# Optimization experiments

Measured on AMD Instinct MI355X. Metric: run time of the kernel, lower is better.

The kernel has to match this reference:

```python
import jax, jax.numpy as jnp
import numpy as np

D = 256      # cfg.d_model
H = 8        # num heads
HID = D // H # head_outdim for hidden layers (32)
N = 16000    # nodes
E = 64000    # edges
NUM_GNN = 3  # cfg.num_gnn -> 2 hidden EGATConv layers + 1 final
SLOPE = 0.01 # F.leaky_relu default in DGL EGATConv


def setup_inputs() -> dict:
    key = jax.random.key(0)
    ks = jax.random.split(key, 8)
    inp = {
        "nfeat": jax.random.normal(ks[0], (N, D), jnp.float32),
        "efeat": jax.random.normal(ks[1], (E, D), jnp.float32),
        "src": jax.random.randint(ks[2], (E,), 0, N),
        "dst": jax.random.randint(ks[3], (E,), 0, N),
    }
    L = NUM_GNN - 1  # hidden layers, out_node = out_edge = HID per head
    kh = jax.random.split(ks[4], 5)
    s = 0.02
    inp["Wnode_h"] = jax.random.normal(kh[0], (L, D, H * HID), jnp.float32) * s
    inp["Wni_h"]   = jax.random.normal(kh[1], (L, D, H * HID), jnp.float32) * s
    inp["Wnj_h"]   = jax.random.normal(kh[2], (L, D, H * HID), jnp.float32) * s
    inp["Wfij_h"]  = jax.random.normal(kh[3], (L, D, H * HID), jnp.float32) * s
    inp["attn_h"]  = jax.random.normal(kh[4], (L, H, HID), jnp.float32) * s
    inp["bias_h"]  = jnp.zeros((L, H * HID), jnp.float32)
    kl = jax.random.split(ks[5], 5)
    inp["Wnode_l"] = jax.random.normal(kl[0], (D, H * D), jnp.float32) * s
    inp["Wni_l"]   = jax.random.normal(kl[1], (D, H * D), jnp.float32) * s
    inp["Wnj_l"]   = jax.random.normal(kl[2], (D, H * D), jnp.float32) * s
    inp["Wfij_l"]  = jax.random.normal(kl[3], (D, H * D), jnp.float32) * s
    inp["attn_l"]  = jax.random.normal(kl[4], (H, D), jnp.float32) * s
    inp["bias_l"]  = jnp.zeros((H * D,), jnp.float32)
    return inp


def _egat(n, f, src, dst, Wnode, Wni, Wnj, Wfij, attn, bias):
    """DGL EGATConv: edge-gated multi-head graph attention.
    n:[N,D] f:[E,D] attn:[H,od] -> (h_out:[N,H,od], f_out:[E,H,od])."""
    Hh, od = attn.shape
    # edge feature update: f_ni(u) + f_nj(v) + f_fij(e) + bias, leaky_relu
    f_out = (n @ Wni)[src] + (n @ Wnj)[dst] + f @ Wfij + bias  # [E, H*od]
    f_out = jax.nn.leaky_relu(f_out, SLOPE).reshape(-1, Hh, od)
    # attention logits + edge softmax grouped by destination node
    e = jnp.einsum('ehd,hd->eh', f_out, attn)                   # [E, H]
    m = jax.lax.stop_gradient(jax.ops.segment_max(e, dst, num_segments=N))
    ex = jnp.exp(e - m[dst])
    s = jax.ops.segment_sum(ex, dst, num_segments=N)
    a = ex / s[dst]                                             # [E, H]
    # message passing: u_mul_e + sum at dst
    h = (n @ Wnode).reshape(N, Hh, od)
    h_out = jax.ops.segment_sum(h[src] * a[..., None], dst, num_segments=N)
    return h_out, f_out


def reference(nfeat, efeat, src, dst,
              Wnode_h, Wni_h, Wnj_h, Wfij_h, attn_h, bias_h,
              Wnode_l, Wni_l, Wnj_l, Wfij_l, attn_l, bias_l):
    n, f = nfeat, efeat
    for l in range(Wnode_h.shape[0]):  # hidden layers: concat heads + ELU + residual
        tn, tf = _egat(n, f, src, dst, Wnode_h[l], Wni_h[l], Wnj_h[l],
                       Wfij_h[l], attn_h[l], bias_h[l])
        n = n + jax.nn.elu(tn.reshape(N, -1))  # reshape == concat over heads
        f = f + jax.nn.elu(tf.reshape(E, -1))
    # last layer: mean over heads + residual
    tn, tf = _egat(n, f, src, dst, Wnode_l, Wni_l, Wnj_l, Wfij_l, attn_l, bias_l)
    n = n + tn.mean(axis=1)
    f = f + tf.mean(axis=1)
    return n, f
```

## Files before the change

### kernel.cpp

```cpp
#include <hip/hip_runtime.h>

typedef unsigned short u16;
typedef __attribute__((ext_vector_type(4))) unsigned short u16x4;
typedef __attribute__((ext_vector_type(8))) unsigned short u16x8;
typedef __attribute__((ext_vector_type(4))) float f32x4;
typedef __attribute__((ext_vector_type(8))) __bf16 bf16x8;

#define NN 16000
#define NE 64000

__device__ __forceinline__ float bf2f(u16 b) {
  union { unsigned int u; float f; } v; v.u = ((unsigned int)b) << 16; return v.f;
}
__device__ __forceinline__ u16 f2bf(float x) {
  union { float f; unsigned int u; } v; v.f = x;
  unsigned int r = v.u + 0x7FFFu + ((v.u >> 16) & 1u);
  return (u16)(r >> 16);
}

__global__ void cast_init(const float* __restrict__ in, float* __restrict__ outf,
                          u16* __restrict__ outb, int n4) {
  for (int i = blockIdx.x * blockDim.x + threadIdx.x; i < n4; i += gridDim.x * blockDim.x) {
    f32x4 v = ((const f32x4*)in)[i];
    u16x4 b;
#pragma unroll
    for (int j = 0; j < 4; ++j) b[j] = f2bf(v[j]);
    ((f32x4*)outf)[i] = v;
    ((u16x4*)outb)[i] = b;
  }
}

__global__ void cast_bf(const float* __restrict__ in, u16* __restrict__ outb, int n4) {
  for (int i = blockIdx.x * blockDim.x + threadIdx.x; i < n4; i += gridDim.x * blockDim.x) {
    f32x4 v = ((const f32x4*)in)[i];
    u16x4 b;
#pragma unroll
    for (int j = 0; j < 4; ++j) b[j] = f2bf(v[j]);
    ((u16x4*)outb)[i] = b;
  }
}

__global__ void deg_hist(const int* __restrict__ dst, int* __restrict__ deg) {
  int e = blockIdx.x * 256 + threadIdx.x;
  if (e < NE) atomicAdd(&deg[dst[e]], 1);
}

__global__ __launch_bounds__(1024) void scan_deg(const int* __restrict__ deg,
                                                 int* __restrict__ row_ptr,
                                                 int* __restrict__ cursor) {
  __shared__ int lds[1024];
  int t = threadIdx.x;
  int base = t * 16;
  int v[16];
  int s = 0;
#pragma unroll
  for (int j = 0; j < 16; ++j) {
    int idx = base + j;
    v[j] = idx < NN ? deg[idx] : 0;
    s += v[j];
  }
  lds[t] = s;
  __syncthreads();
  for (int d = 1; d < 1024; d <<= 1) {
    int x = t >= d ? lds[t - d] : 0;
    __syncthreads();
    lds[t] += x;
    __syncthreads();
  }
  int run = lds[t] - s;
  for (int j = 0; j < 16; ++j) {
    int idx = base + j;
    if (idx < NN) { row_ptr[idx] = run; cursor[idx] = run; run += v[j]; }
  }
  if (t == 1023) row_ptr[NN] = run;
}

__global__ void csr_fill(const int* __restrict__ src, const int* __restrict__ dst,
                         int* __restrict__ cursor, int* __restrict__ cs_e,
                         int* __restrict__ cs_src) {
  int e = blockIdx.x * 256 + threadIdx.x;
  if (e >= NE) return;
  int pos = atomicAdd(&cursor[dst[e]], 1);
  cs_e[pos] = e;
  cs_src[pos] = src[e];
}

__global__ void transpose4(const float* __restrict__ W0, const float* __restrict__ W1,
                           const float* __restrict__ W2, const float* __restrict__ W3,
                           int ld, int osz, u16* __restrict__ WT) {
  __shared__ float t[16][17];
  int z = blockIdx.z;
  const float* W = z == 0 ? W0 : (z == 1 ? W1 : (z == 2 ? W2 : W3));
  u16* O = WT + (size_t)z * osz;
  int n0 = blockIdx.x * 16, k0 = blockIdx.y * 16;
  int tx = threadIdx.x, ty = threadIdx.y;
  t[ty][tx] = W[(size_t)(k0 + ty) * ld + n0 + tx];
  __syncthreads();
  O[(size_t)(n0 + ty) * 256 + k0 + tx] = f2bf(t[tx][ty]);
}

__global__ __launch_bounds__(256) void gemm_abt(
    const u16* __restrict__ A,
    const u16* __restrict__ BT0, const u16* __restrict__ BT1, const u16* __restrict__ BT2,
    u16* __restrict__ C0, u16* __restrict__ C1, u16* __restrict__ C2, int ldc) {
  const int bz = blockIdx.z;
  const u16* BT = bz == 0 ? BT0 : (bz == 1 ? BT1 : BT2);
  u16* C = bz == 0 ? C0 : (bz == 1 ? C1 : C2);
  const int nx = gridDim.x;
  const int nwg = nx * gridDim.y;
  int bid = blockIdx.y * nx + blockIdx.x;
  int q = nwg >> 3, r = nwg & 7;
  int xcd = bid & 7, idx = bid >> 3;
  int wg = (xcd < r) ? (xcd * (q + 1) + idx) : (r * (q + 1) + (xcd - r) * q + idx);
  const int m0 = (wg / nx) * 128;
  const int n0 = (wg % nx) * 128;
  __shared__ __attribute__((aligned(16))) char smem[69632];
  u16* lA = (u16*)smem;
  u16* lB = (u16*)(smem + 32768);
  const int tid = threadIdx.x;
  const int lane = tid & 63;
  const int wid = tid >> 6;
  const int wr = (wid >> 1) * 64;
  const int wc = (wid & 1) * 64;
  const int srow = tid >> 3;
  const int sdst = (tid & 7) * 8;
  const int ssrc = (((tid & 7) ^ (srow & 7))) * 8;
  const int sx = (lane >> 4) ^ (lane & 7);
  f32x4 acc[4][4] = {};
#define STAGE(buf, kb)                                                                         \
  {                                                                                            \
    _Pragma("unroll") for (int i = 0; i < 4; ++i) {                                            \
      const int row = srow + i * 32;                                                           \
      __builtin_amdgcn_global_load_lds(                                                        \
          (const __attribute__((address_space(1))) void*)(A + (size_t)(m0 + row) * 256 + (kb) + ssrc), \
          (__attribute__((address_space(3))) void*)(lA + (buf) * 8192 + row * 64 + sdst), 16, 0, 0); \
      __builtin_amdgcn_global_load_lds(                                                        \
          (const __attribute__((address_space(1))) void*)(BT + (size_t)(n0 + row) * 256 + (kb) + ssrc), \
          (__attribute__((address_space(3))) void*)(lB + (buf) * 8192 + row * 64 + sdst), 16, 0, 0); \
    }                                                                                          \
  }
  STAGE(0, 0)
  __syncthreads();
#pragma unroll
  for (int t = 0; t < 4; ++t) {
    if (t < 3) STAGE((t + 1) & 1, (t + 1) * 64)
    const u16* pA = lA + (t & 1) * 8192;
    const u16* pB = lB + (t & 1) * 8192;
#pragma unroll
    for (int kk = 0; kk < 2; ++kk) {
      const int sw = ((kk << 2) ^ sx) * 8;
      bf16x8 af[4], bfr[4];
#pragma unroll
      for (int m = 0; m < 4; ++m)
        af[m] = *(const bf16x8*)(pA + (wr + m * 16 + (lane & 15)) * 64 + sw);
#pragma unroll
      for (int n = 0; n < 4; ++n)
        bfr[n] = *(const bf16x8*)(pB + (wc + n * 16 + (lane & 15)) * 64 + sw);
#pragma unroll
      for (int m = 0; m < 4; ++m)
#pragma unroll
        for (int n = 0; n < 4; ++n)
          acc[m][n] = __builtin_amdgcn_mfma_f32_16x16x32_bf16(af[m], bfr[n], acc[m][n], 0, 0, 0);
    }
    __syncthreads();
  }
#undef STAGE
  const int cr = (lane >> 4) * 4;
  const int cc = lane & 15;
  float* stg = (float*)smem + wid * (64 * 68);
#pragma unroll
  for (int m = 0; m < 4; ++m)
#pragma unroll
    for (int n = 0; n < 4; ++n)
#pragma unroll
      for (int j = 0; j < 4; ++j)
        stg[(m * 16 + cr + j) * 68 + n * 16 + cc] = acc[m][n][j];
  const int rr = lane >> 3;
  const int c0 = (lane & 7) * 8;
#pragma unroll
  for (int p = 0; p < 8; ++p) {
    int row = p * 8 + rr;
    f32x4 v0 = *(const f32x4*)(stg + row * 68 + c0);
    f32x4 v1 = *(const f32x4*)(stg + row * 68 + c0 + 4);
    u16x8 o;
#pragma unroll
    for (int i = 0; i < 4; ++i) { o[i] = f2bf(v0[i]); o[4 + i] = f2bf(v1[i]); }
    *(u16x8*)(&C[(size_t)(m0 + wr + row) * ldc + (n0 + wc + c0)]) = o;
  }
}

__global__ __launch_bounds__(256) void edge_hidden(
    const u16* __restrict__ t_ni, const u16* __restrict__ t_nj, const u16* __restrict__ fW,
    const int* __restrict__ src, const int* __restrict__ dst,
    const float* __restrict__ bias, const float* __restrict__ attn,
    u16* __restrict__ f_bf, float* __restrict__ exb) {
  int e = blockIdx.x * 4 + (threadIdx.x >> 6);
  if (e >= NE) return;
  int lane = threadIdx.x & 63;
  int is = src[e], id = dst[e];
  int c = lane * 4;
  u16x4 va = *(const u16x4*)(t_ni + (size_t)is * 256 + c);
  u16x4 vb = *(const u16x4*)(t_nj + (size_t)id * 256 + c);
  u16x4 vc = *(const u16x4*)(fW + (size_t)e * 256 + c);
  f32x4 vbi = *(const f32x4*)(bias + c);
  int h = lane >> 3;
  f32x4 vat = *(const f32x4*)(attn + h * 32 + (lane & 7) * 4);
  size_t idx0 = (size_t)e * 256 + c;
  u16x4 fo = *(u16x4*)(f_bf + idx0);
  float part = 0.f;
#pragma unroll
  for (int j = 0; j < 4; ++j) {
    float y = bf2f(va[j]) + bf2f(vb[j]) + bf2f(vc[j]) + vbi[j];
    y = y > 0.f ? y : 0.01f * y;
    part += y * vat[j];
    float el = y > 0.f ? y : expm1f(y);
    fo[j] = f2bf(bf2f(fo[j]) + el);
  }
  *(u16x4*)(f_bf + idx0) = fo;
  part += __shfl_xor(part, 1);
  part += __shfl_xor(part, 2);
  part += __shfl_xor(part, 4);
  part = fminf(fmaxf(part, -30.f), 30.f);
  if ((lane & 7) == 0) exb[(size_t)e * 8 + h] = expf(part);
}

__global__ __launch_bounds__(256) void node_gather_hidden(
    const u16* __restrict__ t_node, const int* __restrict__ row_ptr,
    const int* __restrict__ cs_e, const int* __restrict__ cs_src,
    const float* __restrict__ exb, float* __restrict__ n_cur, u16* __restrict__ n_bf) {
  int node = blockIdx.x * 4 + (threadIdx.x >> 6);
  if (node >= NN) return;
  int lane = threadIdx.x & 63;
  int c = lane * 4, h = lane >> 3;
  int beg = row_ptr[node], end = row_ptr[node + 1];
  float denom = 0.f;
  float acc[4] = {0.f, 0.f, 0.f, 0.f};
  for (int p = beg; p < end; ++p) {
    float a = exb[(size_t)cs_e[p] * 8 + h];
    denom += a;
    u16x4 hv = *(const u16x4*)(t_node + (size_t)cs_src[p] * 256 + c);
#pragma unroll
    for (int j = 0; j < 4; ++j) acc[j] += a * bf2f(hv[j]);
  }
  float inv = denom > 0.f ? 1.f / denom : 0.f;
  size_t i0 = (size_t)node * 256 + c;
  f32x4 nv = *(f32x4*)(n_cur + i0);
  u16x4 bv;
#pragma unroll
  for (int j = 0; j < 4; ++j) {
    float t = acc[j] * inv;
    t = t > 0.f ? t : expm1f(t);
    nv[j] += t;
    bv[j] = f2bf(nv[j]);
  }
  *(f32x4*)(n_cur + i0) = nv;
  *(u16x4*)(n_bf + i0) = bv;
}

__global__ __launch_bounds__(256) void edge_final_all(
    int e0, int nech, const u16* __restrict__ t_ni, const u16* __restrict__ t_nj,
    const u16* __restrict__ fWc, const int* __restrict__ src, const int* __restrict__ dst,
    const float* __restrict__ bias, const float* __restrict__ attn,
    const u16* __restrict__ f_bf, float* __restrict__ out_f, float* __restrict__ exb) {
  int ec = blockIdx.x * 4 + (threadIdx.x >> 6);
  if (ec >= nech) return;
  int e = e0 + ec;
  int lane = threadIdx.x & 63;
  int is = src[e], id = dst[e];
  int c = lane * 4;
  float total[4] = {0.f, 0.f, 0.f, 0.f};
#pragma unroll
  for (int h = 0; h < 8; ++h) {
    u16x4 va = *(const u16x4*)(t_ni + (size_t)is * 2048 + h * 256 + c);
    u16x4 vb = *(const u16x4*)(t_nj + (size_t)id * 2048 + h * 256 + c);
    u16x4 vc = *(const u16x4*)(fWc + (size_t)ec * 2048 + h * 256 + c);
    f32x4 vbi = *(const f32x4*)(bias + h * 256 + c);
    f32x4 vat = *(const f32x4*)(attn + h * 256 + c);
    float part = 0.f;
#pragma unroll
    for (int j = 0; j < 4; ++j) {
      float y = bf2f(va[j]) + bf2f(vb[j]) + bf2f(vc[j]) + vbi[j];
      y = y > 0.f ? y : 0.01f * y;
      part += y * vat[j];
      total[j] += 0.125f * y;
    }
#pragma unroll
    for (int m = 1; m < 64; m <<= 1) part += __shfl_xor(part, m);
    part = fminf(fmaxf(part, -30.f), 30.f);
    if (lane == 0) exb[(size_t)e * 8 + h] = expf(part);
  }
  size_t i0 = (size_t)e * 256 + c;
  u16x4 fs = *(const u16x4*)(f_bf + i0);
  f32x4 o;
#pragma unroll
  for (int j = 0; j < 4; ++j) o[j] = bf2f(fs[j]) + total[j];
  *(f32x4*)(out_f + i0) = o;
}

__global__ __launch_bounds__(256) void node_gather_final_all(
    const u16* __restrict__ t_node, const int* __restrict__ row_ptr,
    const int* __restrict__ cs_e, const int* __restrict__ cs_src,
    const float* __restrict__ exb, const float* __restrict__ n_cur,
    float* __restrict__ out_n) {
  int node = blockIdx.x * 4 + (threadIdx.x >> 6);
  if (node >= NN) return;
  int lane = threadIdx.x & 63;
  int c = lane * 4;
  int beg = row_ptr[node], end = row_ptr[node + 1];
  float dh[8] = {};
  float acc[8][4] = {};
  for (int p = beg; p < end; ++p) {
    int e = cs_e[p];
    int s = cs_src[p];
    const u16* rowb = t_node + (size_t)s * 2048;
    const float* eb = exb + (size_t)e * 8;
    float a[8];
    u16x4 rv[8];
#pragma unroll
    for (int h = 0; h < 8; ++h) {
      a[h] = eb[h];
      rv[h] = *(const u16x4*)(rowb + h * 256 + c);
    }
#pragma unroll
    for (int h = 0; h < 8; ++h) {
      dh[h] += a[h];
#pragma unroll
      for (int j = 0; j < 4; ++j) acc[h][j] += a[h] * bf2f(rv[h][j]);
    }
  }
  float total[4] = {0.f, 0.f, 0.f, 0.f};
#pragma unroll
  for (int h = 0; h < 8; ++h) {
    float inv = dh[h] > 0.f ? 0.125f / dh[h] : 0.f;
#pragma unroll
    for (int j = 0; j < 4; ++j) total[j] += acc[h][j] * inv;
  }
  size_t i0 = (size_t)node * 256 + c;
  f32x4 nv = *(const f32x4*)(n_cur + i0);
#pragma unroll
  for (int j = 0; j < 4; ++j) nv[j] += total[j];
  *(f32x4*)(out_n + i0) = nv;
}

extern "C" void kernel_launch(void* const* d_in, const int* in_sizes, int n_in,
                              void* d_out, int out_size, void* d_ws, size_t ws_size,
                              hipStream_t stream) {
  const float* nfeat   = (const float*)d_in[0];
  const float* efeat   = (const float*)d_in[1];
  const int*   src     = (const int*)d_in[2];
  const int*   dst     = (const int*)d_in[3];
  const float* Wnode_h = (const float*)d_in[4];
  const float* Wni_h   = (const float*)d_in[5];
  const float* Wnj_h   = (const float*)d_in[6];
  const float* Wfij_h  = (const float*)d_in[7];
  const float* attn_h  = (const float*)d_in[8];
  const float* bias_h  = (const float*)d_in[9];
  const float* Wnode_l = (const float*)d_in[10];
  const float* Wni_l   = (const float*)d_in[11];
  const float* Wnj_l   = (const float*)d_in[12];
  const float* Wfij_l  = (const float*)d_in[13];
  const float* attn_l  = (const float*)d_in[14];
  const float* bias_l  = (const float*)d_in[15];

  char* ws = (char*)d_ws;
  size_t off = 0;
  auto alloc = [&](size_t b) { char* p = ws + off; off += (b + 255) & ~(size_t)255; return p; };
  float* n_cur = (float*)alloc((size_t)NN * 256 * 4);
  u16* n_bf    = (u16*)alloc((size_t)NN * 256 * 2);
  u16* f_bf    = (u16*)alloc((size_t)NE * 256 * 2);
  u16* t_ni    = (u16*)alloc((size_t)NN * 2048 * 2);
  u16* t_nj    = (u16*)alloc((size_t)NN * 2048 * 2);
  u16* t_node  = (u16*)alloc((size_t)NN * 2048 * 2);
  float* exb   = (float*)alloc((size_t)NE * 8 * 4);
  u16* WT      = (u16*)alloc((size_t)4 * 65536 * 2);
  u16* WTF     = (u16*)alloc((size_t)4 * 524288 * 2);
  int* deg     = (int*)alloc((size_t)NN * 4);
  int* cursor  = (int*)alloc((size_t)NN * 4);
  int* row_ptr = (int*)alloc((size_t)(NN + 1) * 4);
  int* cs_e    = (int*)alloc((size_t)NE * 4);
  int* cs_src  = (int*)alloc((size_t)NE * 4);
  int ech;
  u16* fW;
  size_t fw_big = (size_t)16000 * 2048 * 2;
  size_t fw_small = (size_t)NE * 256 * 2;
  if (off + fw_big <= ws_size) { ech = 16000; fW = (u16*)alloc(fw_big); }
  else                         { ech = 6400;  fW = (u16*)alloc(fw_small); }

  u16* WT_node = WT;
  u16* WT_ni   = WT + 65536;
  u16* WT_nj   = WT + 2 * 65536;
  u16* WT_fij  = WT + 3 * 65536;
  u16* WTF_node = WTF;
  u16* WTF_ni   = WTF + (size_t)1 * 524288;
  u16* WTF_nj   = WTF + (size_t)2 * 524288;
  u16* WTF_fij  = WTF + (size_t)3 * 524288;

  float* out_n = (float*)d_out;
  float* out_f = out_n + (size_t)NN * 256;

  hipMemsetAsync(deg, 0, (size_t)NN * 4, stream);
  deg_hist<<<(NE + 255) / 256, 256, 0, stream>>>(dst, deg);
  scan_deg<<<1, 1024, 0, stream>>>(deg, row_ptr, cursor);
  csr_fill<<<(NE + 255) / 256, 256, 0, stream>>>(src, dst, cursor, cs_e, cs_src);

  cast_init<<<1024, 256, 0, stream>>>(nfeat, n_cur, n_bf, NN * 256 / 4);
  cast_bf<<<2048, 256, 0, stream>>>(efeat, f_bf, NE * 256 / 4);

  for (int l = 0; l < 2; ++l) {
    transpose4<<<dim3(16, 16, 4), dim3(16, 16), 0, stream>>>(
        Wnode_h + (size_t)l * 65536, Wni_h + (size_t)l * 65536,
        Wnj_h + (size_t)l * 65536, Wfij_h + (size_t)l * 65536, 256, 65536, WT);
    gemm_abt<<<dim3(2, 125, 3), 256, 0, stream>>>(n_bf, WT_ni, WT_nj, WT_node,
                                                  t_ni, t_nj, t_node, 256);
    gemm_abt<<<dim3(2, 500, 1), 256, 0, stream>>>(f_bf, WT_fij, WT_fij, WT_fij,
                                                  fW, fW, fW, 256);
    edge_hidden<<<16000, 256, 0, stream>>>(t_ni, t_nj, fW, src, dst,
        bias_h + (size_t)l * 256, attn_h + (size_t)l * 256, f_bf, exb);
    node_gather_hidden<<<4000, 256, 0, stream>>>(t_node, row_ptr, cs_e, cs_src, exb, n_cur, n_bf);
  }

  transpose4<<<dim3(128, 16, 4), dim3(16, 16), 0, stream>>>(
      Wnode_l, Wni_l, Wnj_l, Wfij_l, 2048, 524288, WTF);
  gemm_abt<<<dim3(16, 125, 3), 256, 0, stream>>>(n_bf, WTF_ni, WTF_nj, WTF_node,
                                                 t_ni, t_nj, t_node, 2048);
  for (int e0 = 0; e0 < NE; e0 += ech) {
    const u16* Ac = f_bf + (size_t)e0 * 256;
    gemm_abt<<<dim3(16, ech / 128, 1), 256, 0, stream>>>(Ac, WTF_fij, WTF_fij, WTF_fij,
                                                         fW, fW, fW, 2048);
    edge_final_all<<<ech / 4, 256, 0, stream>>>(e0, ech, t_ni, t_nj, fW, src, dst,
                                                bias_l, attn_l, f_bf, out_f, exb);
  }
  node_gather_final_all<<<4000, 256, 0, stream>>>(t_node, row_ptr, cs_e, cs_src,
                                                  exb, n_cur, out_n);
}
```

Baseline: 669.1 us.

## Shrink GEMM LDS tiles to K=32 and write outputs directly from registers

The bf16 GEMM now stages K in 32-wide slices instead of 64, cutting shared memory from about 68KB to 32KB per block and requesting 4 blocks per CU through launch bounds. The MFMA operand order is swapped so each lane holds four consecutive output columns, which lets results be written straight from registers as 8-byte stores without the LDS staging epilogue. The aim is higher occupancy and less epilogue LDS traffic, at the cost of twice as many K iterations and barriers, narrower global stores, and possible register pressure under the tighter bound.

```diff
diff --git a/kernel.cpp b/kernel.cpp
--- a/kernel.cpp
+++ b/kernel.cpp
@@ -99,7 +99,7 @@
   O[(size_t)(n0 + ty) * 256 + k0 + tx] = f2bf(t[tx][ty]);
 }
 
-__global__ __launch_bounds__(256) void gemm_abt(
+__global__ __launch_bounds__(256, 4) void gemm_abt(
     const u16* __restrict__ A,
     const u16* __restrict__ BT0, const u16* __restrict__ BT1, const u16* __restrict__ BT2,
     u16* __restrict__ C0, u16* __restrict__ C1, u16* __restrict__ C2, int ldc) {
@@ -114,79 +114,63 @@
   int wg = (xcd < r) ? (xcd * (q + 1) + idx) : (r * (q + 1) + (xcd - r) * q + idx);
   const int m0 = (wg / nx) * 128;
   const int n0 = (wg % nx) * 128;
-  __shared__ __attribute__((aligned(16))) char smem[69632];
-  u16* lA = (u16*)smem;
-  u16* lB = (u16*)(smem + 32768);
+  __shared__ u16 lA[2][128 * 32];
+  __shared__ u16 lB[2][128 * 32];
   const int tid = threadIdx.x;
   const int lane = tid & 63;
   const int wid = tid >> 6;
   const int wr = (wid >> 1) * 64;
   const int wc = (wid & 1) * 64;
-  const int srow = tid >> 3;
-  const int sdst = (tid & 7) * 8;
-  const int ssrc = (((tid & 7) ^ (srow & 7))) * 8;
-  const int sx = (lane >> 4) ^ (lane & 7);
+  const int srow = tid >> 2;
+  const int sdst = (tid & 3) * 8;
+  const int ssrc = ((tid & 3) ^ ((tid >> 3) & 3)) * 8;
+  const int rslot = ((lane >> 4) ^ ((lane >> 1) & 3)) * 8;
   f32x4 acc[4][4] = {};
 #define STAGE(buf, kb)                                                                         \
   {                                                                                            \
-    _Pragma("unroll") for (int i = 0; i < 4; ++i) {                                            \
-      const int row = srow + i * 32;                                                           \
+    _Pragma("unroll") for (int i = 0; i < 2; ++i) {                                            \
+      const int row = srow + i * 64;                                                           \
       __builtin_amdgcn_global_load_lds(                                                        \
           (const __attribute__((address_space(1))) void*)(A + (size_t)(m0 + row) * 256 + (kb) + ssrc), \
-          (__attribute__((address_space(3))) void*)(lA + (buf) * 8192 + row * 64 + sdst), 16, 0, 0); \
+          (__attribute__((address_space(3))) void*)(lA[buf] + row * 32 + sdst), 16, 0, 0);     \
       __builtin_amdgcn_global_load_lds(                                                        \
           (const __attribute__((address_space(1))) void*)(BT + (size_t)(n0 + row) * 256 + (kb) + ssrc), \
-          (__attribute__((address_space(3))) void*)(lB + (buf) * 8192 + row * 64 + sdst), 16, 0, 0); \
+          (__attribute__((address_space(3))) void*)(lB[buf] + row * 32 + sdst), 16, 0, 0);     \
     }                                                                                          \
   }
   STAGE(0, 0)
   __syncthreads();
 #pragma unroll
-  for (int t = 0; t < 4; ++t) {
-    if (t < 3) STAGE((t + 1) & 1, (t + 1) * 64)
-    const u16* pA = lA + (t & 1) * 8192;
-    const u16* pB = lB + (t & 1) * 8192;
-#pragma unroll
-    for (int kk = 0; kk < 2; ++kk) {
-      const int sw = ((kk << 2) ^ sx) * 8;
-      bf16x8 af[4], bfr[4];
-#pragma unroll
-      for (int m = 0; m < 4; ++m)
-        af[m] = *(const bf16x8*)(pA + (wr + m * 16 + (lane & 15)) * 64 + sw);
+  for (int t = 0; t < 8; ++t) {
+    if (t < 7) STAGE((t + 1) & 1, (t + 1) * 32)
+    const u16* pA = lA[t & 1];
+    const u16* pB = lB[t & 1];
+    bf16x8 af[4], bfr[4];
+#pragma unroll
+    for (int m = 0; m < 4; ++m)
+      af[m] = *(const bf16x8*)(pA + (wr + m * 16 + (lane & 15)) * 32 + rslot);
+#pragma unroll
+    for (int n = 0; n < 4; ++n)
+      bfr[n] = *(const bf16x8*)(pB + (wc + n * 16 + (lane & 15)) * 32 + rslot);
+#pragma unroll
+    for (int m = 0; m < 4; ++m)
 #pragma unroll
       for (int n = 0; n < 4; ++n)
-        bfr[n] = *(const bf16x8*)(pB + (wc + n * 16 + (lane & 15)) * 64 + sw);
-#pragma unroll
-      for (int m = 0; m < 4; ++m)
-#pragma unroll
-        for (int n = 0; n < 4; ++n)
-          acc[m][n] = __builtin_amdgcn_mfma_f32_16x16x32_bf16(af[m], bfr[n], acc[m][n], 0, 0, 0);
+        acc[m][n] = __builtin_amdgcn_mfma_f32_16x16x32_bf16(bfr[n], af[m], acc[m][n], 0, 0, 0);
+    __syncthreads();
+  }
+#undef STAGE
+  const int crow = lane & 15;
+  const int cc4 = (lane >> 4) * 4;
+#pragma unroll
+  for (int m = 0; m < 4; ++m)
+#pragma unroll
+    for (int n = 0; n < 4; ++n) {
+      u16x4 o;
+#pragma unroll
+      for (int j = 0; j < 4; ++j) o[j] = f2bf(acc[m][n][j]);
+      *(u16x4*)(&C[(size_t)(m0 + wr + m * 16 + crow) * ldc + (n0 + wc + n * 16 + cc4)]) = o;
     }
-    __syncthreads();
-  }
-#undef STAGE
-  const int cr = (lane >> 4) * 4;
-  const int cc = lane & 15;
-  float* stg = (float*)smem + wid * (64 * 68);
-#pragma unroll
-  for (int m = 0; m < 4; ++m)
-#pragma unroll
-    for (int n = 0; n < 4; ++n)
-#pragma unroll
-      for (int j = 0; j < 4; ++j)
-        stg[(m * 16 + cr + j) * 68 + n * 16 + cc] = acc[m][n][j];
-  const int rr = lane >> 3;
-  const int c0 = (lane & 7) * 8;
-#pragma unroll
-  for (int p = 0; p < 8; ++p) {
-    int row = p * 8 + rr;
-    f32x4 v0 = *(const f32x4*)(stg + row * 68 + c0);
-    f32x4 v1 = *(const f32x4*)(stg + row * 68 + c0 + 4);
-    u16x8 o;
-#pragma unroll
-    for (int i = 0; i < 4; ++i) { o[i] = f2bf(v0[i]); o[4 + i] = f2bf(v1[i]); }
-    *(u16x8*)(&C[(size_t)(m0 + wr + row) * ldc + (n0 + wc + c0)]) = o;
-  }
 }
 
 __global__ __launch_bounds__(256) void edge_hidden(
```

Result: slower. 700.4 us (+4.7%).
